# Optimization experiments

Measured on AMD Instinct MI355X. Metric: run time of the kernel, lower is better.

## Reference

```python
import jax, jax.numpy as jnp
import numpy as np

B, S, R, C_M = 1, 512, 256, 256   # batch, n_seq, n_res, msa channels
C_P, C_Z = 32, 128                # projection channels, pair channels


def setup_inputs() -> dict:
    key = jax.random.key(0)
    ks = jax.random.split(key, 8)
    M = jax.random.normal(ks[0], (B, S, R, C_M), dtype=jnp.float32)
    M_mask = jnp.ones((B, S, R), dtype=jnp.float32)
    Z_raw = jnp.zeros((B, R, R, C_Z), dtype=jnp.float32)
    # LayerNorm params
    ln_g = jnp.ones((C_M,), dtype=jnp.float32)
    ln_b = jnp.zeros((C_M,), dtype=jnp.float32)
    # linear_a / linear_b: glorot-uniform init
    lim = float(np.sqrt(6.0 / (C_M + C_P)))
    Wa = jax.random.uniform(ks[1], (C_P, C_M), minval=-lim, maxval=lim, dtype=jnp.float32)
    ba = jnp.zeros((C_P,), dtype=jnp.float32)
    Wb = jax.random.uniform(ks[2], (C_P, C_M), minval=-lim, maxval=lim, dtype=jnp.float32)
    bb = jnp.zeros((C_P,), dtype=jnp.float32)
    # o_linear is zero-initialized in the source; use small random weights so the
    # output is non-trivial for correctness testing (math is identical).
    Wo = jax.random.normal(ks[3], (C_Z, C_P * C_P), dtype=jnp.float32) * 0.02
    bo = jnp.zeros((C_Z,), dtype=jnp.float32)
    return {"M": M, "M_mask": M_mask, "Z_raw": Z_raw, "ln_g": ln_g, "ln_b": ln_b,
            "Wa": Wa, "ba": ba, "Wb": Wb, "bb": bb, "Wo": Wo, "bo": bo}


def _layernorm(x, g, b, eps=1e-5):
    mu = jnp.mean(x, axis=-1, keepdims=True)
    var = jnp.var(x, axis=-1, keepdims=True)
    return (x - mu) * jax.lax.rsqrt(var + eps) * g + b


def reference(M, M_mask, Z_raw, ln_g, ln_b, Wa, ba, Wb, bb, Wo, bo):
    Mn = _layernorm(M, ln_g, ln_b)                      # [b,s,i,c_m]
    mask = M_mask[..., None]                            # [b,s,i,1]
    left = (jnp.einsum('bsic,dc->bsid', Mn, Wa) + ba) * mask   # [b,s,i,d]
    right = (jnp.einsum('bsic,ec->bsie', Mn, Wb) + bb) * mask  # [b,s,j,e]
    # outer-product mean: contract over sequence dim s
    O = jnp.einsum('bsid,bsje->bijde', left, right)     # [b,i,j,d,e]
    b, i, j, d, e = O.shape
    O = O.reshape(b, i, j, d * e)
    Z = jnp.einsum('bijk,zk->bijz', O, Wo) + bo         # [b,i,j,c_z]
    norm = jnp.einsum('bsi,bsj->bij', M_mask, M_mask)[..., None]
    return Z / (1e-3 + norm)
```

## Files before the change

### kernel.cpp

```cpp
#include <hip/hip_runtime.h>
#include <hip/hip_bf16.h>
#include <stdint.h>

#define S_DIM 512
#define R_DIM 256
#define CM 256
#define CP 32
#define CZ 128

typedef __attribute__((ext_vector_type(8))) short bf16x8;
typedef __attribute__((ext_vector_type(4))) float f32x4;
typedef __attribute__((ext_vector_type(16))) float f32x16;
typedef unsigned int u32;

__device__ __forceinline__ float bf2f(unsigned short u) {
  union { u32 i; float f; } v; v.i = ((u32)u) << 16; return v.f;
}
__device__ __forceinline__ unsigned short f2bf(float f) {
  union { float f; u32 i; } v; v.f = f;
  u32 x = v.i;
  u32 r = (x + 0x7FFFu + ((x >> 16) & 1u)) >> 16;
  return (unsigned short)r;
}

__device__ __forceinline__ void gload_lds16(const unsigned short* g, unsigned short* l) {
  __builtin_amdgcn_global_load_lds((const __attribute__((address_space(1))) u32*)(g),
                                   (__attribute__((address_space(3))) u32*)(l), 16, 0, 0);
}

__device__ __forceinline__ void wave_bar() {
  asm volatile("" ::: "memory");
  __builtin_amdgcn_s_barrier();
  asm volatile("" ::: "memory");
}

__global__ __launch_bounds__(256) void
fused_prep_kernel(const float* __restrict__ Wa, const float* __restrict__ ba,
                  const float* __restrict__ Wb, const float* __restrict__ bb,
                  const float* __restrict__ ln_g, const float* __restrict__ ln_b,
                  const float* __restrict__ Wo, const float* __restrict__ mask,
                  unsigned short* __restrict__ wp, float* __restrict__ Ka,
                  float* __restrict__ Ca, unsigned short* __restrict__ Wo_bf,
                  float* __restrict__ scale) {
  const int b = blockIdx.x;
  const int t = threadIdx.x;
  if (b < 64) {
    __shared__ float ska[4], sca[4];
    const int o = b;
    const float* W = (o < 32) ? (Wa + o * CM) : (Wb + (o - 32) * CM);
    float wv = W[t];
    unsigned short bv = f2bf(wv * ln_g[t]);
    wp[o * CM + t] = bv;
    float ka = bf2f(bv);
    float ca = wv * ln_b[t];
    #pragma unroll
    for (int m = 1; m < 64; m <<= 1) {
      ka += __shfl_xor(ka, m);
      ca += __shfl_xor(ca, m);
    }
    if ((t & 63) == 0) { ska[t >> 6] = ka; sca[t >> 6] = ca; }
    __syncthreads();
    if (t == 0) {
      Ka[o] = ska[0] + ska[1] + ska[2] + ska[3];
      Ca[o] = sca[0] + sca[1] + sca[2] + sca[3] + ((o < 32) ? ba[o] : bb[o - 32]);
    }
  } else if (b < 576) {
    int idx = (b - 64) * 256 + t;
    int z = idx >> 10, k = idx & 1023;
    int d = k >> 5, e = k & 31;
    int kp = e * 32 + d;
    Wo_bf[(kp >> 3) * 1024 + z * 8 + (kp & 7)] = f2bf(Wo[idx]);
  } else {
    const int i = b - 576, j = t;
    float sum = 0.f;
    for (int s = 0; s < S_DIM; ++s)
      sum += mask[s * R_DIM + i] * mask[s * R_DIM + j];
    scale[i * R_DIM + j] = 1.0f / (1e-3f + sum);
  }
}

#define K1_ROWS 64
#define XPAD 264
#define OTP 72

__global__ __launch_bounds__(256) void
ln_proj_kernel(const float* __restrict__ M, const float* __restrict__ mask,
               const unsigned short* __restrict__ wp_g, const float* __restrict__ Ka_g,
               const float* __restrict__ Ca_g,
               unsigned short* __restrict__ leftT, unsigned short* __restrict__ rightT) {
  __shared__ unsigned short xt[K1_ROWS * XPAD];
  __shared__ unsigned short wp[64 * XPAD];
  __shared__ unsigned short ot[64 * OTP];
  __shared__ float smu[K1_ROWS], srs[K1_ROWS], smk[K1_ROWS];
  __shared__ float sKa[64], sCa[64];

  const int t = threadIdx.x;
  const int lane = t & 63;
  const int w = t >> 6;
  const int lm = lane & 15;
  const int rr = lane >> 4;
  const int i = blockIdx.x;
  const int s0 = blockIdx.y * K1_ROWS;

  for (int idx = t; idx < 64 * CM / 8; idx += 256) {
    int row = idx >> 5;
    int col = (idx & 31) * 8;
    *(uint4*)(&wp[row * XPAD + col]) = *(const uint4*)(wp_g + row * CM + col);
  }
  if (t < 64) { sKa[t] = Ka_g[t]; sCa[t] = Ca_g[t]; }

  #pragma unroll
  for (int it = 0; it < 4; ++it) {
    const int row = w * 16 + it * 4 + rr;
    const int sg = s0 + row;
    const float* src = M + ((size_t)sg * R_DIM + i) * CM;
    float4 x[4];
    #pragma unroll
    for (int ch = 0; ch < 4; ++ch) x[ch] = *(const float4*)(src + ch * 64 + lm * 4);
    float sum = 0.f, ssq = 0.f;
    #pragma unroll
    for (int ch = 0; ch < 4; ++ch) {
      sum += x[ch].x + x[ch].y + x[ch].z + x[ch].w;
      ssq += x[ch].x * x[ch].x + x[ch].y * x[ch].y + x[ch].z * x[ch].z + x[ch].w * x[ch].w;
    }
    #pragma unroll
    for (int m = 1; m < 16; m <<= 1) {
      sum += __shfl_xor(sum, m);
      ssq += __shfl_xor(ssq, m);
    }
    float mu = sum * (1.0f / CM);
    float var = ssq * (1.0f / CM) - mu * mu;
    float rs = rsqrtf(var + 1e-5f);
    if (lm == 0) {
      smu[row] = mu; srs[row] = rs;
      smk[row] = mask[(size_t)sg * R_DIM + i];
    }
    #pragma unroll
    for (int ch = 0; ch < 4; ++ch) {
      ushort4 xb;
      xb.x = f2bf(x[ch].x); xb.y = f2bf(x[ch].y); xb.z = f2bf(x[ch].z); xb.w = f2bf(x[ch].w);
      *(ushort4*)(&xt[row * XPAD + ch * 64 + lm * 4]) = xb;
    }
  }
  __syncthreads();

  f32x4 acc[4] = {{0.f, 0.f, 0.f, 0.f}, {0.f, 0.f, 0.f, 0.f},
                  {0.f, 0.f, 0.f, 0.f}, {0.f, 0.f, 0.f, 0.f}};
  #pragma unroll
  for (int k = 0; k < 8; ++k) {
    const int c0 = k * 32 + ((lane >> 4) << 3);
    bf16x8 a = *(const bf16x8*)(&wp[(w * 16 + (lane & 15)) * XPAD + c0]);
    #pragma unroll
    for (int nt = 0; nt < 4; ++nt) {
      bf16x8 b = *(const bf16x8*)(&xt[(nt * 16 + (lane & 15)) * XPAD + c0]);
      acc[nt] = __builtin_amdgcn_mfma_f32_16x16x32_bf16(a, b, acc[nt], 0, 0, 0);
    }
  }

  #pragma unroll
  for (int nt = 0; nt < 4; ++nt) {
    int srow = nt * 16 + (lane & 15);
    float mu = smu[srow], rs = srs[srow], mk = smk[srow];
    #pragma unroll
    for (int r = 0; r < 4; ++r) {
      int o = w * 16 + ((lane >> 4) << 2) + r;
      float v = (rs * (acc[nt][r] - mu * sKa[o]) + sCa[o]) * mk;
      ot[o * OTP + srow] = f2bf(v);
    }
  }
  __syncthreads();

  #pragma unroll
  for (int rep = 0; rep < 2; ++rep) {
    int idx = rep * 256 + t;
    int o = idx >> 3, sg = idx & 7;
    ushort4 lo = *(const ushort4*)(&ot[o * OTP + sg * 8]);
    ushort4 hi = *(const ushort4*)(&ot[o * OTP + sg * 8 + 4]);
    size_t dst = (size_t)(blockIdx.y * 8 + sg) * 65536;
    uint4 v; v.x = (u32)lo.x | ((u32)lo.y << 16); v.y = (u32)lo.z | ((u32)lo.w << 16);
    v.z = (u32)hi.x | ((u32)hi.y << 16); v.w = (u32)hi.z | ((u32)hi.w << 16);
    if (o < 32) *(uint4*)(leftT + dst + (size_t)(i * 32 + o) * 8) = v;
    else        *(uint4*)(rightT + dst + (size_t)(i * 32 + (o - 32)) * 8) = v;
  }
}

#define NT2 8

__global__ __launch_bounds__(512, 1) void
opm_gemm_kernel(const unsigned short* __restrict__ leftT, const unsigned short* __restrict__ rightT,
                const unsigned short* __restrict__ Wo_bf, const float* __restrict__ bo,
                const float* __restrict__ scale, float* __restrict__ out) {
  extern __shared__ unsigned short smem[];

  const int t = threadIdx.x;
  const int lane = t & 63;
  const int lm = lane & 15, lq = lane >> 4;
  const int l31 = lane & 31, lq2 = lane >> 5;
  const int w = t >> 6;
  const int wm = w >> 2, wn = w & 3;

  const int bid = blockIdx.x;
  const int xcd = bid & 7, local = bid >> 3;
  const int by = xcd * 4 + (local & 3);
  const int bx = local >> 2;

  const unsigned short* Asrc = leftT + (size_t)(by * 256) * 8;
  const unsigned short* Bsrc = rightT + (size_t)(bx * 256) * 8;

  int goff[4], ldso[4];
  #pragma unroll
  for (int q = 0; q < 4; ++q) {
    int c = q * 512 + t;
    goff[q] = (c >> 8) * 65536 + (c & 255) * 8;
    ldso[q] = c * 8;
  }

  f32x4 acc[8][4];
  #pragma unroll
  for (int a = 0; a < 8; ++a)
    #pragma unroll
    for (int b = 0; b < 4; ++b) acc[a][b] = (f32x4){0.f, 0.f, 0.f, 0.f};

  auto STAGE = [&](int kt, int buf) {
    const size_t kb = (size_t)kt * 8 * 65536;
    unsigned short* ab = smem + buf * 32768;
    #pragma unroll
    for (int q = 0; q < 4; ++q) {
      gload_lds16(Asrc + kb + goff[q], ab + ldso[q]);
      gload_lds16(Bsrc + kb + goff[q], ab + 16384 + ldso[q]);
    }
  };

  STAGE(0, 0);
  STAGE(1, 1);

  const int abase = lq * 2048 + (wm * 128 + lm) * 8;
  const int bbase = 16384 + lq * 2048 + (wn * 64 + lm) * 8;

  #pragma unroll
  for (int kt = 0; kt < NT2; ++kt) {
    if (kt < NT2 - 1) asm volatile("s_waitcnt vmcnt(8)" ::: "memory");
    else              asm volatile("s_waitcnt vmcnt(0)" ::: "memory");
    wave_bar();

    const unsigned short* Ab = smem + (kt & 1) * 32768;
    #pragma unroll
    for (int ks = 0; ks < 2; ++ks) {
      bf16x8 af[8], bfr[4];
      #pragma unroll
      for (int mi = 0; mi < 8; ++mi)
        af[mi] = *(const bf16x8*)(&Ab[abase + ks * 8192 + mi * 128]);
      #pragma unroll
      for (int ni = 0; ni < 4; ++ni)
        bfr[ni] = *(const bf16x8*)(&Ab[bbase + ks * 8192 + ni * 128]);
      #pragma unroll
      for (int mi = 0; mi < 8; ++mi)
        #pragma unroll
        for (int ni = 0; ni < 4; ++ni)
          acc[mi][ni] = __builtin_amdgcn_mfma_f32_16x16x32_bf16(af[mi], bfr[ni], acc[mi][ni], 0, 0, 0);
    }

    wave_bar();
    if (kt + 2 < NT2) STAGE(kt + 2, kt & 1);
  }

  #pragma unroll
  for (int mi = 0; mi < 8; ++mi) {
    const int m0 = wm * 128 + mi * 16 + lq * 4;
    const int il = m0 >> 5, d0 = m0 & 31;
    #pragma unroll
    for (int ni = 0; ni < 4; ++ni) {
      const int n = wn * 64 + ni * 16 + lm;
      const int jl = n >> 5, e = n & 31;
      const int pair = il * 8 + jl;
      const int kg = e * 4 + (d0 >> 3);
      const u32 byte = (u32)kg * 1024 + (u32)((pair ^ (kg >> 2) ^ (kg & 3)) * 16 + (d0 & 4) * 2);
      ushort4 v4;
      v4.x = f2bf(acc[mi][ni][0]); v4.y = f2bf(acc[mi][ni][1]);
      v4.z = f2bf(acc[mi][ni][2]); v4.w = f2bf(acc[mi][ni][3]);
      *(ushort4*)((char*)smem + byte) = v4;
    }
  }
  __syncthreads();

  f32x16 zacc;
  #pragma unroll
  for (int r = 0; r < 16; ++r) zacc[r] = 0.f;
  const unsigned short* wop = Wo_bf + lq2 * 1024 + (size_t)(wn * 32 + l31) * 8;
  #pragma unroll 4
  for (int kk = 0; kk < 64; ++kk) {
    bf16x8 bw = *(const bf16x8*)(wop + kk * 2048);
    const int kg = kk * 2 + lq2;
    const u32 ob = (u32)kg * 1024 + (u32)((((wm * 32 + l31) ^ (kg >> 2) ^ (kg & 3))) * 16);
    bf16x8 oa = *(const bf16x8*)((const char*)smem + ob);
    zacc = __builtin_amdgcn_mfma_f32_32x32x16_bf16(oa, bw, zacc, 0, 0, 0);
  }

  const int z = wn * 32 + l31;
  const float bz = bo[z];
  #pragma unroll
  for (int r = 0; r < 16; ++r) {
    const int pair = wm * 32 + (r & 3) + 8 * (r >> 2) + 4 * lq2;
    const int ig = by * 8 + (pair >> 3), jg = bx * 8 + (pair & 7);
    float v = (zacc[r] + bz) * scale[ig * R_DIM + jg];
    out[((size_t)ig * R_DIM + jg) * CZ + z] = v;
  }
}

extern "C" void kernel_launch(void* const* d_in, const int* in_sizes, int n_in,
                              void* d_out, int out_size, void* d_ws, size_t ws_size,
                              hipStream_t stream) {
  const float* M     = (const float*)d_in[0];
  const float* Mmask = (const float*)d_in[1];
  const float* ln_g  = (const float*)d_in[3];
  const float* ln_b  = (const float*)d_in[4];
  const float* Wa    = (const float*)d_in[5];
  const float* ba    = (const float*)d_in[6];
  const float* Wb    = (const float*)d_in[7];
  const float* bb    = (const float*)d_in[8];
  const float* Wo    = (const float*)d_in[9];
  const float* bo    = (const float*)d_in[10];
  float* out = (float*)d_out;

  char* ws = (char*)d_ws;
  unsigned short* leftT  = (unsigned short*)(ws);
  unsigned short* rightT = (unsigned short*)(ws + 8388608);
  unsigned short* wp     = (unsigned short*)(ws + 16777216);
  float*          Ka     = (float*)(ws + 16810240);
  float*          Ca     = (float*)(ws + 16810496);
  unsigned short* Wo_bf  = (unsigned short*)(ws + 16810752);
  float*          scale  = (float*)(ws + 17072896);
  (void)ws_size; (void)in_sizes; (void)n_in; (void)out_size;

  hipFuncSetAttribute((const void*)opm_gemm_kernel,
                      hipFuncAttributeMaxDynamicSharedMemorySize, 131072);

  hipLaunchKernelGGL(fused_prep_kernel, dim3(832), dim3(256), 0, stream,
                     Wa, ba, Wb, bb, ln_g, ln_b, Wo, Mmask, wp, Ka, Ca, Wo_bf, scale);
  hipLaunchKernelGGL(ln_proj_kernel, dim3(R_DIM, S_DIM / K1_ROWS), dim3(256), 0, stream,
                     M, Mmask, wp, Ka, Ca, leftT, rightT);
  hipLaunchKernelGGL(opm_gemm_kernel, dim3(1024), dim3(512), 131072, stream,
                     leftT, rightT, Wo_bf, bo, scale, out);
}
```

Measured before the change: 166.8 us.

## Split GEMM k-tile into half-stage loads with interleaved MFMA phases and priority

Restructures the main GEMM loop of the outer-product kernel. Each k-tile is loaded in two halves, and the next tile's halves are issued as soon as the matching half of the current buffer has been read into registers. The compute is split into four smaller MFMA phases, each separated by barriers and wrapped in s_setprio raises. The aim is to overlap global-to-LDS loads with MFMA work more finely and cut register pressure from fragments. In exchange it adds many more barriers per iteration and depends on getting the vmcnt accounting right.

Result: no change. 168.6 us (+1.1%).

```diff
diff --git a/kernel.cpp b/kernel.cpp
--- a/kernel.cpp
+++ b/kernel.cpp
@@ -26,12 +26,6 @@
 __device__ __forceinline__ void gload_lds16(const unsigned short* g, unsigned short* l) {
   __builtin_amdgcn_global_load_lds((const __attribute__((address_space(1))) u32*)(g),
                                    (__attribute__((address_space(3))) u32*)(l), 16, 0, 0);
-}
-
-__device__ __forceinline__ void wave_bar() {
-  asm volatile("" ::: "memory");
-  __builtin_amdgcn_s_barrier();
-  asm volatile("" ::: "memory");
 }
 
 __global__ __launch_bounds__(256) void
@@ -207,61 +201,106 @@
   const unsigned short* Asrc = leftT + (size_t)(by * 256) * 8;
   const unsigned short* Bsrc = rightT + (size_t)(bx * 256) * 8;
 
-  int goff[4], ldso[4];
-  #pragma unroll
-  for (int q = 0; q < 4; ++q) {
-    int c = q * 512 + t;
-    goff[q] = (c >> 8) * 65536 + (c & 255) * 8;
-    ldso[q] = c * 8;
-  }
-
   f32x4 acc[8][4];
   #pragma unroll
   for (int a = 0; a < 8; ++a)
     #pragma unroll
     for (int b = 0; b < 4; ++b) acc[a][b] = (f32x4){0.f, 0.f, 0.f, 0.f};
 
-  auto STAGE = [&](int kt, int buf) {
-    const size_t kb = (size_t)kt * 8 * 65536;
-    unsigned short* ab = smem + buf * 32768;
-    #pragma unroll
-    for (int q = 0; q < 4; ++q) {
-      gload_lds16(Asrc + kb + goff[q], ab + ldso[q]);
-      gload_lds16(Bsrc + kb + goff[q], ab + 16384 + ldso[q]);
+  auto STAGE_U = [&](int kt, int h) {
+    unsigned short* dst = smem + (kt & 1) * 32768;
+    const size_t gp = (size_t)(kt * 8 + h * 4) * 65536;
+    #pragma unroll
+    for (int q = 0; q < 2; ++q) {
+      int c = q * 512 + t;
+      int pi = c >> 8, row = c & 255;
+      gload_lds16(Asrc + gp + (size_t)pi * 65536 + row * 8,
+                  dst + (h * 4 + pi) * 2048 + row * 8);
+      gload_lds16(Bsrc + gp + (size_t)pi * 65536 + row * 8,
+                  dst + 16384 + (h * 4 + pi) * 2048 + row * 8);
     }
   };
 
-  STAGE(0, 0);
-  STAGE(1, 1);
-
-  const int abase = lq * 2048 + (wm * 128 + lm) * 8;
-  const int bbase = 16384 + lq * 2048 + (wn * 64 + lm) * 8;
+  STAGE_U(0, 0);
+  STAGE_U(0, 1);
+  asm volatile("s_waitcnt vmcnt(4)" ::: "memory");
+  __builtin_amdgcn_s_barrier();
+
+  bf16x8 afr[4], bfr[4];
 
   #pragma unroll
   for (int kt = 0; kt < NT2; ++kt) {
-    if (kt < NT2 - 1) asm volatile("s_waitcnt vmcnt(8)" ::: "memory");
-    else              asm volatile("s_waitcnt vmcnt(0)" ::: "memory");
-    wave_bar();
-
     const unsigned short* Ab = smem + (kt & 1) * 32768;
-    #pragma unroll
-    for (int ks = 0; ks < 2; ++ks) {
-      bf16x8 af[8], bfr[4];
-      #pragma unroll
-      for (int mi = 0; mi < 8; ++mi)
-        af[mi] = *(const bf16x8*)(&Ab[abase + ks * 8192 + mi * 128]);
+    const unsigned short* Bb = Ab + 16384;
+    const int aB = (wm * 128 + lm) * 8;
+    const int bB = (wn * 64 + lm) * 8;
+
+    #pragma unroll
+    for (int mi = 0; mi < 4; ++mi)
+      afr[mi] = *(const bf16x8*)(&Ab[lq * 2048 + aB + mi * 128]);
+    #pragma unroll
+    for (int ni = 0; ni < 4; ++ni)
+      bfr[ni] = *(const bf16x8*)(&Bb[lq * 2048 + bB + ni * 128]);
+    if (kt + 1 < NT2) STAGE_U(kt + 1, 0);
+    __builtin_amdgcn_s_barrier();
+    asm volatile("s_waitcnt lgkmcnt(0)" ::: "memory");
+    __builtin_amdgcn_s_setprio(1);
+    #pragma unroll
+    for (int mi = 0; mi < 4; ++mi)
       #pragma unroll
       for (int ni = 0; ni < 4; ++ni)
-        bfr[ni] = *(const bf16x8*)(&Ab[bbase + ks * 8192 + ni * 128]);
+        acc[mi][ni] = __builtin_amdgcn_mfma_f32_16x16x32_bf16(afr[mi], bfr[ni], acc[mi][ni], 0, 0, 0);
+    __builtin_amdgcn_s_setprio(0);
+    __builtin_amdgcn_s_barrier();
+
+    #pragma unroll
+    for (int mi = 0; mi < 4; ++mi)
+      afr[mi] = *(const bf16x8*)(&Ab[lq * 2048 + aB + (4 + mi) * 128]);
+    __builtin_amdgcn_s_barrier();
+    asm volatile("s_waitcnt lgkmcnt(0)" ::: "memory");
+    __builtin_amdgcn_s_setprio(1);
+    #pragma unroll
+    for (int mi = 0; mi < 4; ++mi)
       #pragma unroll
-      for (int mi = 0; mi < 8; ++mi)
-        #pragma unroll
-        for (int ni = 0; ni < 4; ++ni)
-          acc[mi][ni] = __builtin_amdgcn_mfma_f32_16x16x32_bf16(af[mi], bfr[ni], acc[mi][ni], 0, 0, 0);
-    }
-
-    wave_bar();
-    if (kt + 2 < NT2) STAGE(kt + 2, kt & 1);
+      for (int ni = 0; ni < 4; ++ni)
+        acc[4 + mi][ni] = __builtin_amdgcn_mfma_f32_16x16x32_bf16(afr[mi], bfr[ni], acc[4 + mi][ni], 0, 0, 0);
+    __builtin_amdgcn_s_setprio(0);
+    if (kt == NT2 - 1) asm volatile("s_waitcnt vmcnt(0)" ::: "memory");
+    else               asm volatile("s_waitcnt vmcnt(4)" ::: "memory");
+    __builtin_amdgcn_s_barrier();
+
+    #pragma unroll
+    for (int mi = 0; mi < 4; ++mi)
+      afr[mi] = *(const bf16x8*)(&Ab[(4 + lq) * 2048 + aB + mi * 128]);
+    #pragma unroll
+    for (int ni = 0; ni < 4; ++ni)
+      bfr[ni] = *(const bf16x8*)(&Bb[(4 + lq) * 2048 + bB + ni * 128]);
+    if (kt + 1 < NT2) STAGE_U(kt + 1, 1);
+    __builtin_amdgcn_s_barrier();
+    asm volatile("s_waitcnt lgkmcnt(0)" ::: "memory");
+    __builtin_amdgcn_s_setprio(1);
+    #pragma unroll
+    for (int mi = 0; mi < 4; ++mi)
+      #pragma unroll
+      for (int ni = 0; ni < 4; ++ni)
+        acc[mi][ni] = __builtin_amdgcn_mfma_f32_16x16x32_bf16(afr[mi], bfr[ni], acc[mi][ni], 0, 0, 0);
+    __builtin_amdgcn_s_setprio(0);
+    __builtin_amdgcn_s_barrier();
+
+    #pragma unroll
+    for (int mi = 0; mi < 4; ++mi)
+      afr[mi] = *(const bf16x8*)(&Ab[(4 + lq) * 2048 + aB + (4 + mi) * 128]);
+    __builtin_amdgcn_s_barrier();
+    asm volatile("s_waitcnt lgkmcnt(0)" ::: "memory");
+    __builtin_amdgcn_s_setprio(1);
+    #pragma unroll
+    for (int mi = 0; mi < 4; ++mi)
+      #pragma unroll
+      for (int ni = 0; ni < 4; ++ni)
+        acc[4 + mi][ni] = __builtin_amdgcn_mfma_f32_16x16x32_bf16(afr[mi], bfr[ni], acc[4 + mi][ni], 0, 0, 0);
+    __builtin_amdgcn_s_setprio(0);
+    if (kt + 1 < NT2) asm volatile("s_waitcnt vmcnt(4)" ::: "memory");
+    __builtin_amdgcn_s_barrier();
   }
 
   #pragma unroll
```
